# Performance work log

Hardware: AMD Instinct MI355X
Metric: run time of the kernel (lower is better)

Reference implementation:

```python
import jax, jax.numpy as jnp
import numpy as np

DIM = 512; H = 8; DH = 64; M = 256; ITERS = 6; K = 33  # residual conv kernel


def _pinv(x, iters=ITERS):
    # Moore-Penrose iterative pseudo-inverse (lucidrains moore_penrose_iter_pinv)
    abs_x = jnp.abs(x)
    denom = abs_x.sum(-1).max() * abs_x.sum(-2).max()  # global max of col/row sums
    z = jnp.swapaxes(x, -1, -2) / denom
    I = jnp.eye(x.shape[-1], dtype=x.dtype)
    for _ in range(iters):
        xz = x @ z
        z = 0.25 * z @ (13. * I - xz @ (15. * I - xz @ (7. * I - xz)))
    return z


def setup_inputs() -> dict:
    key = jax.random.key(0)
    ks = jax.random.split(key, 5)
    b, n = 4, 4096
    inner = H * DH
    x = jax.random.normal(ks[0], (b, n, DIM), jnp.float32)
    ln_g = jnp.ones((DIM,), jnp.float32)
    ln_b = jnp.zeros((DIM,), jnp.float32)
    w_qkv = jax.random.normal(ks[1], (DIM, 3 * inner), jnp.float32) / np.sqrt(DIM).astype(np.float32)
    w_out = jax.random.normal(ks[2], (inner, DIM), jnp.float32) / np.sqrt(inner).astype(np.float32)
    b_out = jnp.zeros((DIM,), jnp.float32)
    res_w = jax.random.normal(ks[3], (H, K), jnp.float32) * 0.02  # depthwise conv weight per head
    return {"x": x, "ln_g": ln_g, "ln_b": ln_b, "w_qkv": w_qkv,
            "w_out": w_out, "b_out": b_out, "res_w": res_w}


def reference(x, ln_g, ln_b, w_qkv, w_out, b_out, res_w):
    b, n, d = x.shape
    # LayerNorm (eps=1e-5, biased variance, like torch)
    mu = x.mean(-1, keepdims=True)
    var = ((x - mu) ** 2).mean(-1, keepdims=True)
    xn = (x - mu) * jax.lax.rsqrt(var + 1e-5) * ln_g + ln_b
    # QKV projection, no bias
    qkv = xn @ w_qkv  # [b, n, 3*h*dh]
    q, k, v = jnp.split(qkv, 3, axis=-1)
    tohd = lambda t: t.reshape(b, n, H, DH).transpose(0, 2, 1, 3)  # b h n d
    q = tohd(q) * (DH ** -0.5)
    k = tohd(k)
    v = tohd(v)
    # landmarks: mean over consecutive blocks of l = n // M (n divisible by M here)
    l = n // M
    q_l = q.reshape(b, H, M, l, DH).mean(3)  # b h m d
    k_l = k.reshape(b, H, M, l, DH).mean(3)
    attn1 = jax.nn.softmax(jnp.einsum('bhid,bhjd->bhij', q, k_l), axis=-1)   # b h n m
    attn2 = jax.nn.softmax(jnp.einsum('bhid,bhjd->bhij', q_l, k_l), axis=-1)  # b h m m
    attn3 = jax.nn.softmax(jnp.einsum('bhid,bhjd->bhij', q_l, k), axis=-1)   # b h m n
    out = (attn1 @ _pinv(attn2)) @ (attn3 @ v)  # b h n dh
    # depthwise residual conv over sequence dim (Conv2d(heads, heads, (33,1), groups=heads))
    res = jax.lax.conv_general_dilated(
        v, res_w.reshape(H, 1, K, 1), (1, 1), ((K // 2, K // 2), (0, 0)),
        feature_group_count=H, dimension_numbers=('NCHW', 'OIHW', 'NCHW'))
    out = out + res
    # merge heads + output projection (dropout is identity at eval)
    out = out.transpose(0, 2, 1, 3).reshape(b, n, H * DH) @ w_out + b_out
    # TransLayer residual
    return x + out
```

## Files before the change

kernel.cpp:

```cpp
#include <hip/hip_runtime.h>
#include <hip/hip_bf16.h>

#define SEQ    4096
#define NBAT   4
#define NHEAD  8
#define NBH    32
#define DMODEL 512
#define DHEAD  64
#define NLM    256
#define NSP    4

typedef __attribute__((ext_vector_type(8))) short s8v;
typedef __attribute__((ext_vector_type(4))) float f4v;

__device__ __forceinline__ float b2f(unsigned short u){
  union { unsigned int i; float f; } v; v.i = ((unsigned int)u) << 16; return v.f;
}
__device__ __forceinline__ unsigned short f2b(float f){
  union { float f; unsigned int i; } v; v.f = f;
  unsigned int r = v.i + 0x7fffu + ((v.i >> 16) & 1u);
  return (unsigned short)(r >> 16);
}
__device__ __forceinline__ s8v ldg8(const unsigned short* p){
  return *reinterpret_cast<const s8v*>(p);
}
__device__ __forceinline__ f4v mfma16(s8v a, s8v b, f4v c){
  return __builtin_amdgcn_mfma_f32_16x16x32_bf16(a, b, c, 0, 0, 0);
}
__device__ __forceinline__ f4v zero4(){ f4v z; z[0]=0.f; z[1]=0.f; z[2]=0.f; z[3]=0.f; return z; }
__device__ __forceinline__ void gload16(const unsigned short* g, unsigned short* l){
  __builtin_amdgcn_global_load_lds((const __attribute__((address_space(1))) unsigned int*)g,
                                   (__attribute__((address_space(3))) unsigned int*)l, 16, 0, 0);
}

__global__ void k_prep(const float* __restrict__ wqkv, const float* __restrict__ wout,
                       unsigned short* __restrict__ wqkvT, unsigned short* __restrict__ woutT,
                       unsigned int* __restrict__ denomU){
  int t = blockIdx.x*256 + threadIdx.x;
  if (t == 0) denomU[0] = 0u;
  if (t < 786432){ int kk = t/1536, n = t%1536; wqkvT[(size_t)n*512 + kk] = f2b(wqkv[t]); }
  else { int t2 = t - 786432; if (t2 < 262144){ int kk = t2/512, n = t2%512; woutT[(size_t)n*512 + kk] = f2b(wout[t2]); } }
}

__global__ __launch_bounds__(256) void k_ln(const float* __restrict__ x, const float* __restrict__ g,
                                            const float* __restrict__ be, unsigned short* __restrict__ xn){
  int row = blockIdx.x*4 + (threadIdx.x>>6);
  int l = threadIdx.x & 63;
  const float* xr = x + (size_t)row*DMODEL;
  float4 a = *(const float4*)(xr + l*4);
  float4 b = *(const float4*)(xr + 256 + l*4);
  float s = a.x+a.y+a.z+a.w + b.x+b.y+b.z+b.w;
  float q = a.x*a.x+a.y*a.y+a.z*a.z+a.w*a.w + b.x*b.x+b.y*b.y+b.z*b.z+b.w*b.w;
  #pragma unroll
  for (int m=1;m<64;m<<=1){ s += __shfl_xor(s,m); q += __shfl_xor(q,m); }
  float mean = s*(1.f/DMODEL);
  float rstd = rsqrtf(q*(1.f/DMODEL) - mean*mean + 1e-5f);
  int c0 = l*4, c1 = 256 + l*4;
  float av[4] = {a.x,a.y,a.z,a.w}, bv[4] = {b.x,b.y,b.z,b.w};
  ushort4 u0, u1;
  unsigned short* p0 = (unsigned short*)&u0; unsigned short* p1 = (unsigned short*)&u1;
  #pragma unroll
  for (int e=0;e<4;++e){
    p0[e] = f2b((av[e]-mean)*rstd*g[c0+e] + be[c0+e]);
    p1[e] = f2b((bv[e]-mean)*rstd*g[c1+e] + be[c1+e]);
  }
  *(ushort4*)(xn + (size_t)row*DMODEL + c0) = u0;
  *(ushort4*)(xn + (size_t)row*DMODEL + c1) = u1;
}

__device__ __forceinline__ void gemm512v2(const unsigned short* __restrict__ A, const unsigned short* __restrict__ B,
                                          int m0, int n0, int t, unsigned short* lA, unsigned short* lB,
                                          f4v acc[4][4]){
  int w = t>>6, l = t&63;
  int wm = (w&1)*64, wn = (w>>1)*64;
  int g = l>>4, qi = l&15;
  int rs = (w<<4) + (l>>2);
  int s0 = l&3;
  int c0 = ((s0 ^ ((rs>>1)&3)) << 3);
  int r1 = rs + 64;
  int c1 = ((s0 ^ ((r1>>1)&3)) << 3);
  const unsigned short* gA0 = A + (size_t)(m0+rs)*DMODEL + c0;
  const unsigned short* gA1 = A + (size_t)(m0+r1)*DMODEL + c1;
  const unsigned short* gB0 = B + (size_t)(n0+rs)*DMODEL + c0;
  const unsigned short* gB1 = B + (size_t)(n0+r1)*DMODEL + c1;
  unsigned short* dA0 = lA + (w<<9);
  unsigned short* dA1 = lA + 2048 + (w<<9);
  unsigned short* dB0 = lB + (w<<9);
  unsigned short* dB1 = lB + 2048 + (w<<9);
  int aofs[4], bofs[4];
  #pragma unroll
  for (int i=0;i<4;++i){
    int ra = wm + i*16 + qi;
    aofs[i] = ra*32 + ((g ^ ((ra>>1)&3))<<3);
    int rb = wn + i*16 + qi;
    bofs[i] = rb*32 + ((g ^ ((rb>>1)&3))<<3);
  }
  for (int ks=0; ks<16; ++ks){
    gload16(gA0, dA0); gload16(gA1, dA1);
    gload16(gB0, dB0); gload16(gB1, dB1);
    gA0 += 32; gA1 += 32; gB0 += 32; gB1 += 32;
    __syncthreads();
    s8v af[4], bf[4];
    #pragma unroll
    for (int i=0;i<4;++i) af[i] = *(s8v*)&lA[aofs[i]];
    #pragma unroll
    for (int j=0;j<4;++j) bf[j] = *(s8v*)&lB[bofs[j]];
    #pragma unroll
    for (int i=0;i<4;++i)
      #pragma unroll
      for (int j=0;j<4;++j) acc[i][j] = mfma16(af[i], bf[j], acc[i][j]);
    __syncthreads();
  }
}

__global__ __launch_bounds__(256) void k_gqkv(const unsigned short* __restrict__ xn, const unsigned short* __restrict__ wT,
                                              unsigned short* __restrict__ q, unsigned short* __restrict__ k,
                                              unsigned short* __restrict__ v, unsigned short* __restrict__ vT){
  __shared__ __align__(16) unsigned short lA[4096], lB[4096];
  int b0 = blockIdx.x;
  int bid = (b0 & 7) * 192 + (b0 >> 3);
  int mblk = bid/12, nblk = bid%12;
  int m0 = mblk*128, n0 = nblk*128;
  int t = threadIdx.x;
  f4v acc[4][4];
  #pragma unroll
  for (int i=0;i<4;++i)
    #pragma unroll
    for (int j=0;j<4;++j) acc[i][j] = zero4();
  gemm512v2(xn, wT, m0, n0, t, lA, lB, acc);
  int w = t>>6, l = t&63; int wm = (w&1)*64, wn = (w>>1)*64;
  int part = nblk >> 2;
  int coff = (nblk & 3) * 128;
  unsigned short* dst = (part==0) ? q : (part==1) ? k : v;
  float scale = (part==0) ? 0.125f : 1.f;
  #pragma unroll
  for (int i=0;i<4;++i)
  #pragma unroll
  for (int j=0;j<4;++j){
    int colg = coff + wn + j*16 + (l&15);
    int h = colg>>6, c = colg&63;
    #pragma unroll
    for (int r=0;r<4;++r){
      int rowg = m0 + wm + i*16 + ((l>>4)<<2) + r;
      int b = rowg>>12, n = rowg&4095;
      unsigned short val = f2b(acc[i][j][r]*scale);
      dst[ (((size_t)(b*NHEAD + h))*SEQ + n)*DHEAD + c ] = val;
      if (part == 2)
        vT[ (((size_t)(b*NHEAD + h))*DHEAD + c)*SEQ + n ] = val;
    }
  }
}

__global__ __launch_bounds__(256) void k_gout(const unsigned short* __restrict__ ao, const unsigned short* __restrict__ wT,
                                              const float* __restrict__ x, const float* __restrict__ bo,
                                              float* __restrict__ out){
  __shared__ __align__(16) unsigned short lA[4096], lB[4096];
  int b0 = blockIdx.x;
  int bid = (b0 & 7) * 64 + (b0 >> 3);
  int mblk = bid>>2, nblk = bid&3;
  int m0 = mblk*128, n0 = nblk*128;
  int t = threadIdx.x;
  f4v acc[4][4];
  #pragma unroll
  for (int i=0;i<4;++i)
    #pragma unroll
    for (int j=0;j<4;++j) acc[i][j] = zero4();
  gemm512v2(ao, wT, m0, n0, t, lA, lB, acc);
  int w = t>>6, l = t&63; int wm = (w&1)*64, wn = (w>>1)*64;
  #pragma unroll
  for (int i=0;i<4;++i)
  #pragma unroll
  for (int j=0;j<4;++j){
    int colg = n0 + wn + j*16 + (l&15);
    #pragma unroll
    for (int r=0;r<4;++r){
      int rowg = m0 + wm + i*16 + ((l>>4)<<2) + r;
      size_t ad = (size_t)rowg*DMODEL + colg;
      out[ad] = acc[i][j][r] + x[ad] + bo[colg];
    }
  }
}

__global__ void k_lmk(const unsigned short* __restrict__ q, const unsigned short* __restrict__ k,
                      unsigned short* __restrict__ ql, unsigned short* __restrict__ kl){
  int tg = blockIdx.x*256 + threadIdx.x;
  int c4 = (tg&15)*4, m = (tg>>4)&255, bh = tg>>12;
  const unsigned short* qb = q + ((size_t)bh*SEQ + m*16)*DHEAD + c4;
  const unsigned short* kb = k + ((size_t)bh*SEQ + m*16)*DHEAD + c4;
  float s0=0.f,s1=0.f,s2=0.f,s3=0.f, t0=0.f,t1=0.f,t2=0.f,t3=0.f;
  #pragma unroll
  for (int j=0;j<16;++j){
    ushort4 uq = *(const ushort4*)(qb + (size_t)j*DHEAD);
    ushort4 uk = *(const ushort4*)(kb + (size_t)j*DHEAD);
    s0+=b2f(uq.x); s1+=b2f(uq.y); s2+=b2f(uq.z); s3+=b2f(uq.w);
    t0+=b2f(uk.x); t1+=b2f(uk.y); t2+=b2f(uk.z); t3+=b2f(uk.w);
  }
  ushort4 oq, ok;
  oq.x=f2b(s0*(1.f/16.f)); oq.y=f2b(s1*(1.f/16.f)); oq.z=f2b(s2*(1.f/16.f)); oq.w=f2b(s3*(1.f/16.f));
  ok.x=f2b(t0*(1.f/16.f)); ok.y=f2b(t1*(1.f/16.f)); ok.z=f2b(t2*(1.f/16.f)); ok.w=f2b(t3*(1.f/16.f));
  *(ushort4*)(ql + ((size_t)bh*NLM + m)*DHEAD + c4) = oq;
  *(ushort4*)(kl + ((size_t)bh*NLM + m)*DHEAD + c4) = ok;
}

__global__ __launch_bounds__(512) void k_attn2(const unsigned short* __restrict__ ql, const unsigned short* __restrict__ kl,
                                               unsigned short* __restrict__ a2, unsigned short* __restrict__ a2t,
                                               unsigned int* __restrict__ denomU){
  __shared__ float cs[256];
  int bh = blockIdx.x; int t = threadIdx.x; int w = t>>6, l = t&63;
  const unsigned short* Q = ql + (size_t)bh*NLM*DHEAD;
  const unsigned short* K = kl + (size_t)bh*NLM*DHEAD;
  f4v acc[2][16];
  #pragma unroll
  for (int i=0;i<2;++i)
    #pragma unroll
    for (int j=0;j<16;++j) acc[i][j] = zero4();
  int m0 = w*32;
  #pragma unroll
  for (int ks=0; ks<2; ++ks){
    int kk = ks*32 + ((l>>4)<<3);
    s8v af0 = ldg8(&Q[(size_t)(m0 + (l&15))*DHEAD + kk]);
    s8v af1 = ldg8(&Q[(size_t)(m0 + 16 + (l&15))*DHEAD + kk]);
    #pragma unroll
    for (int j=0;j<16;++j){
      s8v bf = ldg8(&K[(size_t)(j*16 + (l&15))*DHEAD + kk]);
      acc[0][j] = mfma16(af0, bf, acc[0][j]);
      acc[1][j] = mfma16(af1, bf, acc[1][j]);
    }
  }
  #pragma unroll
  for (int i=0;i<2;++i)
  #pragma unroll
  for (int r=0;r<4;++r){
    float mx = -1e30f;
    #pragma unroll
    for (int j=0;j<16;++j) mx = fmaxf(mx, acc[i][j][r]);
    #pragma unroll
    for (int mm=1;mm<16;mm<<=1) mx = fmaxf(mx, __shfl_xor(mx,mm));
    float sm = 0.f;
    #pragma unroll
    for (int j=0;j<16;++j){ float p = __expf(acc[i][j][r]-mx); acc[i][j][r]=p; sm += p; }
    #pragma unroll
    for (int mm=1;mm<16;mm<<=1) sm += __shfl_xor(sm,mm);
    float inv = 1.f/sm;
    #pragma unroll
    for (int j=0;j<16;++j) acc[i][j][r] *= inv;
  }
  for (int e=t; e<256; e+=512) cs[e] = 0.f;
  __syncthreads();
  size_t b0 = (size_t)bh*NLM*NLM;
  #pragma unroll
  for (int i=0;i<2;++i)
  #pragma unroll
  for (int j=0;j<16;++j){
    int col = j*16 + (l&15);
    int rowb = m0 + i*16 + ((l>>4)<<2);
    float csp = 0.f;
    #pragma unroll
    for (int r=0;r<4;++r){
      float p = acc[i][j][r];
      unsigned short pb = f2b(p);
      a2 [b0 + (size_t)(rowb+r)*NLM + col] = pb;
      a2t[b0 + (size_t)col*NLM + rowb + r] = pb;
      csp += p;
    }
    csp += __shfl_xor(csp, 16); csp += __shfl_xor(csp, 32);
    if ((l>>4) == 0) atomicAdd(&cs[col], csp);
  }
  __syncthreads();
  if (t < 256) atomicMax(denomU, __float_as_uint(cs[t]));
}

__global__ __launch_bounds__(128) void k_a3w2p(const unsigned short* __restrict__ ql, const unsigned short* __restrict__ kb,
                                               const unsigned short* __restrict__ vT,
                                               float* __restrict__ po, float* __restrict__ pm, float* __restrict__ pd){
  int ksp = blockIdx.x & 3;
  int qb  = (blockIdx.x >> 2) & 7;
  int bh  = blockIdx.x >> 5;
  int t = threadIdx.x, w = t>>6, l = t&63;
  int q0 = (qb<<5) + (w<<4);
  int g = l>>4, qi = l&15;
  const unsigned short* Q = ql + ((size_t)bh*NLM + q0)*DHEAD;
  const unsigned short* K = kb + (size_t)bh*SEQ*DHEAD;
  const unsigned short* V = vT + (size_t)bh*DHEAD*SEQ;
  float m_run = -1e30f, den = 0.f;
  f4v oacc[4];
  #pragma unroll
  for (int j=0;j<4;++j) oacc[j] = zero4();
  int sl0 = ((g&1)*2)*16 + qi;
  int jsel = g>>1;
  for (int kc = ksp*4; kc < ksp*4+4; ++kc){
    const unsigned short* Kc = K + (size_t)kc*256*DHEAD;
    f4v acc[16];
    #pragma unroll
    for (int j=0;j<16;++j) acc[j] = zero4();
    #pragma unroll
    for (int ks=0;ks<2;++ks){
      int kk = ks*32 + g*8;
      s8v bq = ldg8(&Q[(size_t)qi*DHEAD + kk]);
      #pragma unroll
      for (int j=0;j<16;++j){
        s8v ak = ldg8(&Kc[(size_t)(j*16+qi)*DHEAD + kk]);
        acc[j] = mfma16(ak, bq, acc[j]);
      }
    }
    float cm = -1e30f;
    #pragma unroll
    for (int j=0;j<16;++j)
      cm = fmaxf(cm, fmaxf(fmaxf(acc[j][0],acc[j][1]), fmaxf(acc[j][2],acc[j][3])));
    cm = fmaxf(cm, __shfl_xor(cm,16));
    cm = fmaxf(cm, __shfl_xor(cm,32));
    float nm = fmaxf(m_run, cm);
    float f = __expf(m_run - nm);
    m_run = nm;
    float ls = 0.f;
    unsigned int pku[32];
    #pragma unroll
    for (int j=0;j<16;++j){
      float p0 = __expf(acc[j][0]-nm), p1 = __expf(acc[j][1]-nm);
      float p2 = __expf(acc[j][2]-nm), p3 = __expf(acc[j][3]-nm);
      ls += (p0+p1)+(p2+p3);
      pku[2*j+0] = (unsigned int)f2b(p0) | ((unsigned int)f2b(p1)<<16);
      pku[2*j+1] = (unsigned int)f2b(p2) | ((unsigned int)f2b(p3)<<16);
    }
    den = den*f + ls;
    float fr0 = __shfl(f, g*4+0, 64), fr1 = __shfl(f, g*4+1, 64);
    float fr2 = __shfl(f, g*4+2, 64), fr3 = __shfl(f, g*4+3, 64);
    #pragma unroll
    for (int j=0;j<4;++j){
      oacc[j][0]*=fr0; oacc[j][1]*=fr1; oacc[j][2]*=fr2; oacc[j][3]*=fr3;
    }
    #pragma unroll
    for (int ks=0;ks<8;++ks){
      unsigned int w0a = (unsigned int)__shfl((int)pku[4*ks+0], sl0, 64);
      unsigned int w1a = (unsigned int)__shfl((int)pku[4*ks+1], sl0, 64);
      unsigned int w0b = (unsigned int)__shfl((int)pku[4*ks+2], sl0, 64);
      unsigned int w1b = (unsigned int)__shfl((int)pku[4*ks+3], sl0, 64);
      unsigned int w2a = (unsigned int)__shfl((int)pku[4*ks+0], sl0+16, 64);
      unsigned int w3a = (unsigned int)__shfl((int)pku[4*ks+1], sl0+16, 64);
      unsigned int w2b = (unsigned int)__shfl((int)pku[4*ks+2], sl0+16, 64);
      unsigned int w3b = (unsigned int)__shfl((int)pku[4*ks+3], sl0+16, 64);
      unsigned int wv0 = jsel ? w0b : w0a;
      unsigned int wv1 = jsel ? w1b : w1a;
      unsigned int wv2 = jsel ? w2b : w2a;
      unsigned int wv3 = jsel ? w3b : w3a;
      s8v af;
      af[0] = (short)(wv0&0xffff); af[1] = (short)(wv0>>16);
      af[2] = (short)(wv1&0xffff); af[3] = (short)(wv1>>16);
      af[4] = (short)(wv2&0xffff); af[5] = (short)(wv2>>16);
      af[6] = (short)(wv3&0xffff); af[7] = (short)(wv3>>16);
      int mk = ks*32 + g*8;
      #pragma unroll
      for (int j=0;j<4;++j){
        s8v bu = ldg8(&V[(size_t)(j*16+qi)*SEQ + kc*256 + mk]);
        oacc[j] = mfma16(af, bu, oacc[j]);
      }
    }
  }
  den += __shfl_xor(den,16); den += __shfl_xor(den,32);
  #pragma unroll
  for (int j=0;j<4;++j)
    #pragma unroll
    for (int r=0;r<4;++r)
      po[(((size_t)(ksp*NBH + bh))*NLM + q0 + g*4 + r)*DHEAD + j*16 + qi] = oacc[j][r];
  if (g == 0){
    pm[(size_t)(ksp*NBH + bh)*NLM + q0 + qi] = m_run;
    pd[(size_t)(ksp*NBH + bh)*NLM + q0 + qi] = den;
  }
}

__global__ __launch_bounds__(256) void k_a3c(const float* __restrict__ po, const float* __restrict__ pm,
                                             const float* __restrict__ pd, unsigned short* __restrict__ w2t){
  int tg = blockIdx.x*256 + threadIdx.x;
  int bh = tg >> 12; int c = (tg >> 6) & 63; int r4 = (tg & 63) << 2;
  ushort4 ov;
  unsigned short* op = (unsigned short*)&ov;
  #pragma unroll
  for (int rr=0; rr<4; ++rr){
    int row = r4 + rr;
    float m[NSP];
    float gm = -1e30f;
    #pragma unroll
    for (int s=0;s<NSP;++s){ m[s] = pm[(size_t)(s*NBH+bh)*NLM + row]; gm = fmaxf(gm, m[s]); }
    float den = 0.f, o = 0.f;
    #pragma unroll
    for (int s=0;s<NSP;++s){
      float wsc = __expf(m[s]-gm);
      den += pd[(size_t)(s*NBH+bh)*NLM + row]*wsc;
      o   += po[(((size_t)(s*NBH+bh))*NLM + row)*DHEAD + c]*wsc;
    }
    op[rr] = f2b(o/den);
  }
  *(ushort4*)&w2t[(size_t)bh*DHEAD*NLM + (size_t)c*NLM + r4] = ov;
}

__global__ __launch_bounds__(256) void k_conv(const unsigned short* __restrict__ v, const float* __restrict__ rw,
                                              unsigned short* __restrict__ cf){
  int bh = blockIdx.x >> 6;
  int n0 = (blockIdx.x & 63) * 64;
  int h = bh & 7, b = bh >> 3;
  int t = threadIdx.x;
  int tx = t & 15, ty = t >> 4;
  int c4 = tx * 4;
  int nb = n0 + ty * 4;
  const unsigned short* vb = v + ((size_t)bh * SEQ) * DHEAD + c4;
  ushort4 val[36];
  #pragma unroll
  for (int i = 0; i < 36; ++i){
    int nn = nb - 16 + i;
    if (nn >= 0 && nn < SEQ) val[i] = *(const ushort4*)(vb + (size_t)nn * DHEAD);
    else { val[i].x = 0; val[i].y = 0; val[i].z = 0; val[i].w = 0; }
  }
  float wgt[33];
  #pragma unroll
  for (int o = 0; o < 33; ++o) wgt[o] = rw[h*33 + o];
  #pragma unroll
  for (int i = 0; i < 4; ++i){
    float s0 = 0.f, s1 = 0.f, s2 = 0.f, s3 = 0.f;
    #pragma unroll
    for (int o = 0; o < 33; ++o){
      ushort4 u = val[i + o];
      float w0 = wgt[o];
      s0 += w0 * b2f(u.x); s1 += w0 * b2f(u.y);
      s2 += w0 * b2f(u.z); s3 += w0 * b2f(u.w);
    }
    ushort4 ov;
    ov.x = f2b(s0); ov.y = f2b(s1); ov.z = f2b(s2); ov.w = f2b(s3);
    size_t ad = ((size_t)b * SEQ + (nb + i)) * DMODEL + h * DHEAD + c4;
    *(ushort4*)(cf + ad) = ov;
  }
}

__device__ __forceinline__ void pcore(const unsigned short* __restrict__ Ab, const unsigned short* __restrict__ Bb,
                                      int m0, int n0, int l, f4v acc[4][4]){
  for (int ks=0; ks<8; ++ks){
    int kk = ks*32 + ((l>>4)<<3);
    s8v af[4], bf[4];
    #pragma unroll
    for (int i=0;i<4;++i) af[i] = ldg8(&Ab[(size_t)(m0 + i*16 + (l&15))*256 + kk]);
    #pragma unroll
    for (int j=0;j<4;++j) bf[j] = ldg8(&Bb[(size_t)(n0 + j*16 + (l&15))*256 + kk]);
    #pragma unroll
    for (int i=0;i<4;++i)
      #pragma unroll
      for (int j=0;j<4;++j) acc[i][j] = mfma16(af[i], bf[j], acc[i][j]);
  }
}

__global__ __launch_bounds__(64) void k_pg1(const unsigned short* __restrict__ A, const unsigned short* __restrict__ BT,
                                            unsigned short* __restrict__ oN, unsigned short* __restrict__ oT,
                                            int sdiv, const unsigned int* __restrict__ denomU){
  int bid = blockIdx.x;
  int bh = bid>>4, tt = bid&15;
  int m0 = (tt>>2)*64, n0 = (tt&3)*64;
  int l = threadIdx.x;
  const unsigned short* Ab = A + (size_t)bh*65536;
  const unsigned short* Bb = BT + (size_t)bh*65536;
  f4v acc[4][4];
  #pragma unroll
  for (int i=0;i<4;++i)
    #pragma unroll
    for (int j=0;j<4;++j) acc[i][j] = zero4();
  pcore(Ab, Bb, m0, n0, l, acc);
  float s = sdiv ? 1.f/__uint_as_float(denomU[0]) : 1.f;
  #pragma unroll
  for (int i=0;i<4;++i)
  #pragma unroll
  for (int j=0;j<4;++j){
    int col = n0 + j*16 + (l&15);
    #pragma unroll
    for (int r=0;r<4;++r){
      int row = m0 + i*16 + ((l>>4)<<2) + r;
      unsigned short ob = f2b(acc[i][j][r]*s);
      oN[(size_t)bh*65536 + (size_t)row*256 + col] = ob;
      oT[(size_t)bh*65536 + (size_t)col*256 + row] = ob;
    }
  }
}

__global__ __launch_bounds__(64) void k_pg2(const unsigned short* __restrict__ xzN, const unsigned short* __restrict__ xzT,
                                            const unsigned short* __restrict__ zsrc,
                                            unsigned short* __restrict__ CT, unsigned short* __restrict__ PN,
                                            int sdiv, const unsigned int* __restrict__ denomU){
  int bid = blockIdx.x;
  int part = bid>>9; bid &= 511;
  int bh = bid>>4, tt = bid&15;
  int m0 = (tt>>2)*64, n0 = (tt&3)*64;
  int l = threadIdx.x;
  const unsigned short* Ab = (part==0 ? xzN : zsrc) + (size_t)bh*65536;
  const unsigned short* Bb = xzT + (size_t)bh*65536;
  f4v acc[4][4];
  #pragma unroll
  for (int i=0;i<4;++i)
    #pragma unroll
    for (int j=0;j<4;++j) acc[i][j] = zero4();
  pcore(Ab, Bb, m0, n0, l, acc);
  if (part == 0){
    #pragma unroll
    for (int i=0;i<4;++i)
    #pragma unroll
    for (int j=0;j<4;++j){
      int col = n0 + j*16 + (l&15);
      #pragma unroll
      for (int r=0;r<4;++r){
        int row = m0 + i*16 + ((l>>4)<<2) + r;
        float xv = b2f(xzN[(size_t)bh*65536 + (size_t)row*256 + col]);
        CT[(size_t)bh*65536 + (size_t)col*256 + row] = f2b(7.f*xv - acc[i][j][r]);
      }
    }
  } else {
    float s = sdiv ? 1.f/__uint_as_float(denomU[0]) : 1.f;
    #pragma unroll
    for (int i=0;i<4;++i)
    #pragma unroll
    for (int j=0;j<4;++j){
      int col = n0 + j*16 + (l&15);
      #pragma unroll
      for (int r=0;r<4;++r){
        int row = m0 + i*16 + ((l>>4)<<2) + r;
        PN[(size_t)bh*65536 + (size_t)row*256 + col] = f2b(acc[i][j][r]*s);
      }
    }
  }
}

__global__ __launch_bounds__(64) void k_pg3(const unsigned short* __restrict__ PN, const unsigned short* __restrict__ CT,
                                            const unsigned short* __restrict__ zsrc,
                                            unsigned short* __restrict__ zN, unsigned short* __restrict__ zT,
                                            int sdiv, const unsigned int* __restrict__ denomU){
  int bid = blockIdx.x;
  int bh = bid>>4, tt = bid&15;
  int m0 = (tt>>2)*64, n0 = (tt&3)*64;
  int l = threadIdx.x;
  const unsigned short* Ab = PN + (size_t)bh*65536;
  const unsigned short* Bb = CT + (size_t)bh*65536;
  f4v acc[4][4];
  #pragma unroll
  for (int i=0;i<4;++i)
    #pragma unroll
    for (int j=0;j<4;++j) acc[i][j] = zero4();
  pcore(Ab, Bb, m0, n0, l, acc);
  float zs = sdiv ? 1.f/__uint_as_float(denomU[0]) : 1.f;
  #pragma unroll
  for (int i=0;i<4;++i)
  #pragma unroll
  for (int j=0;j<4;++j){
    int col = n0 + j*16 + (l&15);
    #pragma unroll
    for (int r=0;r<4;++r){
      int row = m0 + i*16 + ((l>>4)<<2) + r;
      float zv = b2f(zsrc[(size_t)bh*65536 + (size_t)row*256 + col])*zs;
      float pv = b2f(PN  [(size_t)bh*65536 + (size_t)row*256 + col]);
      float res = 0.25f*(13.f*zv - 15.f*pv + acc[i][j][r]);
      unsigned short ob = f2b(res);
      zN[(size_t)bh*65536 + (size_t)row*256 + col] = ob;
      zT[(size_t)bh*65536 + (size_t)col*256 + row] = ob;
    }
  }
}

template<bool WN, bool WT>
__global__ __launch_bounds__(64) void k_pgemm(
    const unsigned short* __restrict__ A, const unsigned short* __restrict__ BT,
    unsigned short* __restrict__ oN, unsigned short* __restrict__ oT,
    int mt, int nt, long strA, long strBT, long strON, long strOT)
{
  int bid = blockIdx.x;
  int nper = mt*nt;
  int bh = bid/nper, tt = bid%nper;
  int m0 = (tt/nt)*64, n0 = (tt%nt)*64;
  const unsigned short* Ab = A + (size_t)bh*strA;
  const unsigned short* Bb = BT + (size_t)bh*strBT;
  int l = threadIdx.x;
  f4v acc[4][4];
  #pragma unroll
  for (int i=0;i<4;++i)
    #pragma unroll
    for (int j=0;j<4;++j) acc[i][j] = zero4();
  pcore(Ab, Bb, m0, n0, l, acc);
  #pragma unroll
  for (int i=0;i<4;++i)
  #pragma unroll
  for (int j=0;j<4;++j){
    int col = n0 + j*16 + (l&15);
    #pragma unroll
    for (int r=0;r<4;++r){
      int row = m0 + i*16 + ((l>>4)<<2) + r;
      unsigned short ob = f2b(acc[i][j][r]);
      if constexpr (WN) oN[(size_t)bh*strON + (size_t)row*256 + col] = ob;
      if constexpr (WT) oT[(size_t)bh*strOT + (size_t)col*256 + row] = ob;
    }
  }
}

__global__ __launch_bounds__(256) void k_attn1(const unsigned short* __restrict__ qb, const unsigned short* __restrict__ kl,
                                               const unsigned short* __restrict__ ut, const unsigned short* __restrict__ cf,
                                               unsigned short* __restrict__ ao){
  int bh = blockIdx.x>>6;
  int t = threadIdx.x, w = t>>6, l = t&63;
  int q0 = ((blockIdx.x&63)<<6) + (w<<4);
  int g = l>>4, qi = l&15;
  const unsigned short* Q = qb + (size_t)bh*SEQ*DHEAD;
  const unsigned short* K = kl + (size_t)bh*NLM*DHEAD;
  f4v acc[16];
  #pragma unroll
  for (int j=0;j<16;++j) acc[j] = zero4();
  #pragma unroll
  for (int ks=0;ks<2;++ks){
    int kk = ks*32 + g*8;
    s8v bq = ldg8(&Q[(size_t)(q0+qi)*DHEAD + kk]);
    #pragma unroll
    for (int j=0;j<16;++j){
      s8v ak = ldg8(&K[(size_t)(j*16+qi)*DHEAD + kk]);
      acc[j] = mfma16(ak, bq, acc[j]);
    }
  }
  float mx = -1e30f;
  #pragma unroll
  for (int j=0;j<16;++j)
    mx = fmaxf(mx, fmaxf(fmaxf(acc[j][0],acc[j][1]), fmaxf(acc[j][2],acc[j][3])));
  mx = fmaxf(mx, __shfl_xor(mx,16));
  mx = fmaxf(mx, __shfl_xor(mx,32));
  float sm = 0.f;
  #pragma unroll
  for (int j=0;j<16;++j)
    #pragma unroll
    for (int r=0;r<4;++r){ float p = __expf(acc[j][r]-mx); acc[j][r]=p; sm += p; }
  sm += __shfl_xor(sm,16); sm += __shfl_xor(sm,32);
  float inv = 1.f/sm;
  unsigned int pku[32];
  #pragma unroll
  for (int j=0;j<16;++j){
    pku[2*j+0] = (unsigned int)f2b(acc[j][0]*inv) | ((unsigned int)f2b(acc[j][1]*inv)<<16);
    pku[2*j+1] = (unsigned int)f2b(acc[j][2]*inv) | ((unsigned int)f2b(acc[j][3]*inv)<<16);
  }
  const unsigned short* U = ut + (size_t)bh*DHEAD*NLM;
  f4v oacc[4];
  #pragma unroll
  for (int j=0;j<4;++j) oacc[j] = zero4();
  int sl0 = ((g&1)*2)*16 + qi;
  int jsel = g>>1;
  #pragma unroll
  for (int ks=0;ks<8;++ks){
    unsigned int w0a = (unsigned int)__shfl((int)pku[4*ks+0], sl0, 64);
    unsigned int w1a = (unsigned int)__shfl((int)pku[4*ks+1], sl0, 64);
    unsigned int w0b = (unsigned int)__shfl((int)pku[4*ks+2], sl0, 64);
    unsigned int w1b = (unsigned int)__shfl((int)pku[4*ks+3], sl0, 64);
    unsigned int w2a = (unsigned int)__shfl((int)pku[4*ks+0], sl0+16, 64);
    unsigned int w3a = (unsigned int)__shfl((int)pku[4*ks+1], sl0+16, 64);
    unsigned int w2b = (unsigned int)__shfl((int)pku[4*ks+2], sl0+16, 64);
    unsigned int w3b = (unsigned int)__shfl((int)pku[4*ks+3], sl0+16, 64);
    unsigned int wv0 = jsel ? w0b : w0a;
    unsigned int wv1 = jsel ? w1b : w1a;
    unsigned int wv2 = jsel ? w2b : w2a;
    unsigned int wv3 = jsel ? w3b : w3a;
    s8v af;
    af[0] = (short)(wv0&0xffff); af[1] = (short)(wv0>>16);
    af[2] = (short)(wv1&0xffff); af[3] = (short)(wv1>>16);
    af[4] = (short)(wv2&0xffff); af[5] = (short)(wv2>>16);
    af[6] = (short)(wv3&0xffff); af[7] = (short)(wv3>>16);
    int mk = ks*32 + g*8;
    #pragma unroll
    for (int j=0;j<4;++j){
      s8v bu = ldg8(&U[(size_t)(j*16+qi)*NLM + mk]);
      oacc[j] = mfma16(af, bu, oacc[j]);
    }
  }
  int b = bh>>3, h = bh&7;
  #pragma unroll
  for (int j=0;j<4;++j){
    int c = j*16 + qi;
    #pragma unroll
    for (int r=0;r<4;++r){
      int n = q0 + g*4 + r;
      size_t ad = ((size_t)(b*SEQ + n))*DMODEL + h*DHEAD + c;
      ao[ad] = f2b(oacc[j][r] + b2f(cf[ad]));
    }
  }
}

extern "C" void kernel_launch(void* const* d_in, const int* in_sizes, int n_in,
                              void* d_out, int out_size, void* d_ws, size_t ws_size,
                              hipStream_t stream){
  const float* x    = (const float*)d_in[0];
  const float* lng  = (const float*)d_in[1];
  const float* lnb  = (const float*)d_in[2];
  const float* wqkv = (const float*)d_in[3];
  const float* wout = (const float*)d_in[4];
  const float* bout = (const float*)d_in[5];
  const float* resw = (const float*)d_in[6];
  float* out = (float*)d_out;

  char* ws = (char*)d_ws;
  size_t off = 0;
  auto alloc = [&](size_t bytes)->char*{ char* p = ws + off; off += (bytes + 255) & ~(size_t)255; return p; };

  unsigned short* wqkvT = (unsigned short*)alloc((size_t)1536*512*2);
  unsigned short* woutT = (unsigned short*)alloc((size_t)512*512*2);
  unsigned int*   denomU= (unsigned int*)  alloc(256);
  unsigned short* xn    = (unsigned short*)alloc((size_t)16384*512*2);
  unsigned short* zA  = xn;
  unsigned short* zAT = xn + (size_t)1*NBH*NLM*NLM;
  unsigned short* zB  = xn + (size_t)2*NBH*NLM*NLM;
  unsigned short* zBT = xn + (size_t)3*NBH*NLM*NLM;
  unsigned short* q   = (unsigned short*)alloc((size_t)NBH*SEQ*DHEAD*2);
  unsigned short* kb  = (unsigned short*)alloc((size_t)NBH*SEQ*DHEAD*2);
  unsigned short* ao  = kb;
  unsigned short* v   = (unsigned short*)alloc((size_t)NBH*SEQ*DHEAD*2);
  unsigned short* vT  = (unsigned short*)alloc((size_t)NBH*DHEAD*SEQ*2);
  unsigned short* ql  = (unsigned short*)alloc((size_t)NBH*NLM*DHEAD*2);
  unsigned short* kl  = (unsigned short*)alloc((size_t)NBH*NLM*DHEAD*2);
  unsigned short* a2  = (unsigned short*)alloc((size_t)NBH*NLM*NLM*2);
  unsigned short* a2t = (unsigned short*)alloc((size_t)NBH*NLM*NLM*2);
  unsigned short* convf = (unsigned short*)alloc((size_t)NBAT*SEQ*DMODEL*2);
  unsigned short* xzN = (unsigned short*)alloc((size_t)NBH*NLM*NLM*2);
  unsigned short* xzT = (unsigned short*)alloc((size_t)NBH*NLM*NLM*2);
  unsigned short* pn  = (unsigned short*)alloc((size_t)NBH*NLM*NLM*2);
  unsigned short* ctb = (unsigned short*)alloc((size_t)NBH*NLM*NLM*2);
  float* po = (float*)alloc((size_t)NSP*NBH*NLM*DHEAD*4);
  float* pm = (float*)alloc((size_t)NSP*NBH*NLM*4);
  float* pd = (float*)alloc((size_t)NSP*NBH*NLM*4);
  unsigned short* w2t = (unsigned short*)alloc((size_t)NBH*DHEAD*NLM*2);
  unsigned short* ut  = (unsigned short*)alloc((size_t)NBH*DHEAD*NLM*2);
  (void)ws_size; (void)in_sizes; (void)n_in; (void)out_size;

  k_prep<<<4096,256,0,stream>>>(wqkv, wout, wqkvT, woutT, denomU);
  k_ln  <<<4096,256,0,stream>>>(x, lng, lnb, xn);
  k_gqkv<<<1536,256,0,stream>>>(xn, wqkvT, q, kb, v, vT);
  k_lmk <<<512,256,0,stream>>>(q, kb, ql, kl);
  k_attn2<<<32,512,0,stream>>>(ql, kl, a2, a2t, denomU);
  k_a3w2p<<<1024,128,0,stream>>>(ql, kb, vT, po, pm, pd);
  k_a3c <<<512,256,0,stream>>>(po, pm, pd, w2t);
  k_conv<<<2048,256,0,stream>>>(v, resw, convf);

  unsigned short* zN_[2] = {zA, zB};
  unsigned short* zT_[2] = {zAT, zBT};
  for (int it = 0; it < 6; ++it){
    const unsigned short* BT   = (it==0) ? a2  : zT_[(it-1)&1];
    const unsigned short* zsrc = (it==0) ? a2t : zN_[(it-1)&1];
    int sdiv = (it==0) ? 1 : 0;
    k_pg1<<<512 ,64,0,stream>>>(a2, BT, xzN, xzT, sdiv, denomU);
    k_pg2<<<1024,64,0,stream>>>(xzN, xzT, zsrc, ctb, pn, sdiv, denomU);
    k_pg3<<<512 ,64,0,stream>>>(pn, ctb, zsrc, zN_[it&1], zT_[it&1], sdiv, denomU);
  }
  k_pgemm<false,true><<<128,64,0,stream>>>(zN_[1], w2t, (unsigned short*)nullptr, ut, 4,1, 65536L,16384L,0L,16384L);

  k_attn1<<<2048,256,0,stream>>>(q, kl, ut, convf, ao);
  k_gout <<<512,256,0,stream>>>(ao, woutT, x, bout, out);
}
```

Before: 497.1 us.

## Fuse pseudo-inverse iterations into one persistent kernel with grid barriers

Replaces the 18 per-iteration GEMM launches plus the final pgemm with a single persistent kernel of 512 blocks that synchronises through atomic-counter grid barriers in global memory. The two GEMMs that were split across 1024 blocks in pg2 are now done back to back by each block. The goal is to remove launch overhead and inter-kernel gaps in the small serial Newton-Schulz chain. In exchange, each block does twice the work in one phase, and the spin barriers rely on all 512 blocks being co-resident, risking deadlock otherwise.

Measured after the change: 1.570 ms. 3.16x slower.

```diff
diff --git a/kernel.cpp b/kernel.cpp
--- a/kernel.cpp
+++ b/kernel.cpp
@@ -35,9 +35,10 @@
 
 __global__ void k_prep(const float* __restrict__ wqkv, const float* __restrict__ wout,
                        unsigned short* __restrict__ wqkvT, unsigned short* __restrict__ woutT,
-                       unsigned int* __restrict__ denomU){
+                       unsigned int* __restrict__ denomU, unsigned int* __restrict__ bar){
   int t = blockIdx.x*256 + threadIdx.x;
   if (t == 0) denomU[0] = 0u;
+  if (t < 64) bar[t] = 0u;
   if (t < 786432){ int kk = t/1536, n = t%1536; wqkvT[(size_t)n*512 + kk] = f2b(wqkv[t]); }
   else { int t2 = t - 786432; if (t2 < 262144){ int kk = t2/512, n = t2%512; woutT[(size_t)n*512 + kk] = f2b(wout[t2]); } }
 }
@@ -446,148 +447,146 @@
   }
 }
 
-__global__ __launch_bounds__(64) void k_pg1(const unsigned short* __restrict__ A, const unsigned short* __restrict__ BT,
-                                            unsigned short* __restrict__ oN, unsigned short* __restrict__ oT,
-                                            int sdiv, const unsigned int* __restrict__ denomU){
+__device__ __forceinline__ void gbar(unsigned int* __restrict__ bar, int ph, int l){
+  __threadfence();
+  if (l == 0) atomicAdd(&bar[ph], 1u);
+  while (__hip_atomic_load(&bar[ph], __ATOMIC_RELAXED, __HIP_MEMORY_SCOPE_AGENT) < 512u)
+    __builtin_amdgcn_s_sleep(8);
+  __threadfence();
+}
+
+__global__ __launch_bounds__(64) void k_pinv(
+    const unsigned short* __restrict__ a2, const unsigned short* __restrict__ a2t,
+    const unsigned short* __restrict__ w2t, unsigned short* __restrict__ ut,
+    unsigned short* __restrict__ xzN, unsigned short* __restrict__ xzT,
+    unsigned short* __restrict__ ctb, unsigned short* __restrict__ pn,
+    unsigned short* __restrict__ zA, unsigned short* __restrict__ zAT,
+    unsigned short* __restrict__ zB, unsigned short* __restrict__ zBT,
+    const unsigned int* __restrict__ denomU, unsigned int* __restrict__ bar)
+{
   int bid = blockIdx.x;
+  int l = threadIdx.x;
   int bh = bid>>4, tt = bid&15;
   int m0 = (tt>>2)*64, n0 = (tt&3)*64;
-  int l = threadIdx.x;
-  const unsigned short* Ab = A + (size_t)bh*65536;
-  const unsigned short* Bb = BT + (size_t)bh*65536;
-  f4v acc[4][4];
-  #pragma unroll
-  for (int i=0;i<4;++i)
-    #pragma unroll
-    for (int j=0;j<4;++j) acc[i][j] = zero4();
-  pcore(Ab, Bb, m0, n0, l, acc);
-  float s = sdiv ? 1.f/__uint_as_float(denomU[0]) : 1.f;
-  #pragma unroll
-  for (int i=0;i<4;++i)
-  #pragma unroll
-  for (int j=0;j<4;++j){
-    int col = n0 + j*16 + (l&15);
-    #pragma unroll
-    for (int r=0;r<4;++r){
-      int row = m0 + i*16 + ((l>>4)<<2) + r;
-      unsigned short ob = f2b(acc[i][j][r]*s);
-      oN[(size_t)bh*65536 + (size_t)row*256 + col] = ob;
-      oT[(size_t)bh*65536 + (size_t)col*256 + row] = ob;
-    }
-  }
-}
-
-__global__ __launch_bounds__(64) void k_pg2(const unsigned short* __restrict__ xzN, const unsigned short* __restrict__ xzT,
-                                            const unsigned short* __restrict__ zsrc,
-                                            unsigned short* __restrict__ CT, unsigned short* __restrict__ PN,
-                                            int sdiv, const unsigned int* __restrict__ denomU){
-  int bid = blockIdx.x;
-  int part = bid>>9; bid &= 511;
-  int bh = bid>>4, tt = bid&15;
-  int m0 = (tt>>2)*64, n0 = (tt&3)*64;
-  int l = threadIdx.x;
-  const unsigned short* Ab = (part==0 ? xzN : zsrc) + (size_t)bh*65536;
-  const unsigned short* Bb = xzT + (size_t)bh*65536;
-  f4v acc[4][4];
-  #pragma unroll
-  for (int i=0;i<4;++i)
-    #pragma unroll
-    for (int j=0;j<4;++j) acc[i][j] = zero4();
-  pcore(Ab, Bb, m0, n0, l, acc);
-  if (part == 0){
+  size_t bb = (size_t)bh*65536;
+  float dinv = 1.f/__uint_as_float(denomU[0]);
+  unsigned short* zN_[2] = {zA, zB};
+  unsigned short* zT_[2] = {zAT, zBT};
+  int ph = 0;
+  for (int it=0; it<6; ++it){
+    const unsigned short* BT   = (it==0) ? a2  : zT_[(it-1)&1];
+    const unsigned short* zsrc = (it==0) ? a2t : zN_[(it-1)&1];
+    float s = (it==0) ? dinv : 1.f;
+    {
+      f4v acc[4][4];
+      #pragma unroll
+      for (int i=0;i<4;++i)
+        #pragma unroll
+        for (int j=0;j<4;++j) acc[i][j] = zero4();
+      pcore(a2+bb, BT+bb, m0, n0, l, acc);
+      #pragma unroll
+      for (int i=0;i<4;++i)
+      #pragma unroll
+      for (int j=0;j<4;++j){
+        int col = n0 + j*16 + (l&15);
+        #pragma unroll
+        for (int r=0;r<4;++r){
+          int row = m0 + i*16 + ((l>>4)<<2) + r;
+          unsigned short ob = f2b(acc[i][j][r]*s);
+          xzN[bb + (size_t)row*256 + col] = ob;
+          xzT[bb + (size_t)col*256 + row] = ob;
+        }
+      }
+    }
+    gbar(bar, ph++, l);
+    {
+      f4v acc[4][4];
+      #pragma unroll
+      for (int i=0;i<4;++i)
+        #pragma unroll
+        for (int j=0;j<4;++j) acc[i][j] = zero4();
+      pcore(xzN+bb, xzT+bb, m0, n0, l, acc);
+      #pragma unroll
+      for (int i=0;i<4;++i)
+      #pragma unroll
+      for (int j=0;j<4;++j){
+        int col = n0 + j*16 + (l&15);
+        #pragma unroll
+        for (int r=0;r<4;++r){
+          int row = m0 + i*16 + ((l>>4)<<2) + r;
+          float xv = b2f(xzN[bb + (size_t)row*256 + col]);
+          ctb[bb + (size_t)col*256 + row] = f2b(7.f*xv - acc[i][j][r]);
+        }
+      }
+    }
+    {
+      f4v acc[4][4];
+      #pragma unroll
+      for (int i=0;i<4;++i)
+        #pragma unroll
+        for (int j=0;j<4;++j) acc[i][j] = zero4();
+      pcore(zsrc+bb, xzT+bb, m0, n0, l, acc);
+      #pragma unroll
+      for (int i=0;i<4;++i)
+      #pragma unroll
+      for (int j=0;j<4;++j){
+        int col = n0 + j*16 + (l&15);
+        #pragma unroll
+        for (int r=0;r<4;++r){
+          int row = m0 + i*16 + ((l>>4)<<2) + r;
+          pn[bb + (size_t)row*256 + col] = f2b(acc[i][j][r]*s);
+        }
+      }
+    }
+    gbar(bar, ph++, l);
+    {
+      f4v acc[4][4];
+      #pragma unroll
+      for (int i=0;i<4;++i)
+        #pragma unroll
+        for (int j=0;j<4;++j) acc[i][j] = zero4();
+      pcore(pn+bb, ctb+bb, m0, n0, l, acc);
+      unsigned short* zdN = zN_[it&1];
+      unsigned short* zdT = zT_[it&1];
+      #pragma unroll
+      for (int i=0;i<4;++i)
+      #pragma unroll
+      for (int j=0;j<4;++j){
+        int col = n0 + j*16 + (l&15);
+        #pragma unroll
+        for (int r=0;r<4;++r){
+          int row = m0 + i*16 + ((l>>4)<<2) + r;
+          size_t idx = bb + (size_t)row*256 + col;
+          float zv = b2f(zsrc[idx])*s;
+          float pv = b2f(pn[idx]);
+          float res = 0.25f*(13.f*zv - 15.f*pv + acc[i][j][r]);
+          unsigned short ob = f2b(res);
+          zdN[idx] = ob;
+          zdT[bb + (size_t)col*256 + row] = ob;
+        }
+      }
+    }
+    gbar(bar, ph++, l);
+  }
+  if (bid < 128){
+    int bh2 = bid>>2, tte = bid&3;
+    int m0e = tte*64;
+    f4v acc[4][4];
     #pragma unroll
     for (int i=0;i<4;++i)
+      #pragma unroll
+      for (int j=0;j<4;++j) acc[i][j] = zero4();
+    pcore(zB + (size_t)bh2*65536, w2t + (size_t)bh2*16384, m0e, 0, l, acc);
+    #pragma unroll
+    for (int i=0;i<4;++i)
     #pragma unroll
     for (int j=0;j<4;++j){
-      int col = n0 + j*16 + (l&15);
+      int col = j*16 + (l&15);
       #pragma unroll
       for (int r=0;r<4;++r){
-        int row = m0 + i*16 + ((l>>4)<<2) + r;
-        float xv = b2f(xzN[(size_t)bh*65536 + (size_t)row*256 + col]);
-        CT[(size_t)bh*65536 + (size_t)col*256 + row] = f2b(7.f*xv - acc[i][j][r]);
+        int row = m0e + i*16 + ((l>>4)<<2) + r;
+        ut[(size_t)bh2*16384 + (size_t)col*256 + row] = f2b(acc[i][j][r]);
       }
-    }
-  } else {
-    float s = sdiv ? 1.f/__uint_as_float(denomU[0]) : 1.f;
-    #pragma unroll
-    for (int i=0;i<4;++i)
-    #pragma unroll
-    for (int j=0;j<4;++j){
-      int col = n0 + j*16 + (l&15);
-      #pragma unroll
-      for (int r=0;r<4;++r){
-        int row = m0 + i*16 + ((l>>4)<<2) + r;
-        PN[(size_t)bh*65536 + (size_t)row*256 + col] = f2b(acc[i][j][r]*s);
-      }
-    }
-  }
-}
-
-__global__ __launch_bounds__(64) void k_pg3(const unsigned short* __restrict__ PN, const unsigned short* __restrict__ CT,
-                                            const unsigned short* __restrict__ zsrc,
-                                            unsigned short* __restrict__ zN, unsigned short* __restrict__ zT,
-                                            int sdiv, const unsigned int* __restrict__ denomU){
-  int bid = blockIdx.x;
-  int bh = bid>>4, tt = bid&15;
-  int m0 = (tt>>2)*64, n0 = (tt&3)*64;
-  int l = threadIdx.x;
-  const unsigned short* Ab = PN + (size_t)bh*65536;
-  const unsigned short* Bb = CT + (size_t)bh*65536;
-  f4v acc[4][4];
-  #pragma unroll
-  for (int i=0;i<4;++i)
-    #pragma unroll
-    for (int j=0;j<4;++j) acc[i][j] = zero4();
-  pcore(Ab, Bb, m0, n0, l, acc);
-  float zs = sdiv ? 1.f/__uint_as_float(denomU[0]) : 1.f;
-  #pragma unroll
-  for (int i=0;i<4;++i)
-  #pragma unroll
-  for (int j=0;j<4;++j){
-    int col = n0 + j*16 + (l&15);
-    #pragma unroll
-    for (int r=0;r<4;++r){
-      int row = m0 + i*16 + ((l>>4)<<2) + r;
-      float zv = b2f(zsrc[(size_t)bh*65536 + (size_t)row*256 + col])*zs;
-      float pv = b2f(PN  [(size_t)bh*65536 + (size_t)row*256 + col]);
-      float res = 0.25f*(13.f*zv - 15.f*pv + acc[i][j][r]);
-      unsigned short ob = f2b(res);
-      zN[(size_t)bh*65536 + (size_t)row*256 + col] = ob;
-      zT[(size_t)bh*65536 + (size_t)col*256 + row] = ob;
-    }
-  }
-}
-
-template<bool WN, bool WT>
-__global__ __launch_bounds__(64) void k_pgemm(
-    const unsigned short* __restrict__ A, const unsigned short* __restrict__ BT,
-    unsigned short* __restrict__ oN, unsigned short* __restrict__ oT,
-    int mt, int nt, long strA, long strBT, long strON, long strOT)
-{
-  int bid = blockIdx.x;
-  int nper = mt*nt;
-  int bh = bid/nper, tt = bid%nper;
-  int m0 = (tt/nt)*64, n0 = (tt%nt)*64;
-  const unsigned short* Ab = A + (size_t)bh*strA;
-  const unsigned short* Bb = BT + (size_t)bh*strBT;
-  int l = threadIdx.x;
-  f4v acc[4][4];
-  #pragma unroll
-  for (int i=0;i<4;++i)
-    #pragma unroll
-    for (int j=0;j<4;++j) acc[i][j] = zero4();
-  pcore(Ab, Bb, m0, n0, l, acc);
-  #pragma unroll
-  for (int i=0;i<4;++i)
-  #pragma unroll
-  for (int j=0;j<4;++j){
-    int col = n0 + j*16 + (l&15);
-    #pragma unroll
-    for (int r=0;r<4;++r){
-      int row = m0 + i*16 + ((l>>4)<<2) + r;
-      unsigned short ob = f2b(acc[i][j][r]);
-      if constexpr (WN) oN[(size_t)bh*strON + (size_t)row*256 + col] = ob;
-      if constexpr (WT) oT[(size_t)bh*strOT + (size_t)col*256 + row] = ob;
     }
   }
 }
@@ -697,6 +696,7 @@
   unsigned short* wqkvT = (unsigned short*)alloc((size_t)1536*512*2);
   unsigned short* woutT = (unsigned short*)alloc((size_t)512*512*2);
   unsigned int*   denomU= (unsigned int*)  alloc(256);
+  unsigned int*   bar   = (unsigned int*)  alloc(256);
   unsigned short* xn    = (unsigned short*)alloc((size_t)16384*512*2);
   unsigned short* zA  = xn;
   unsigned short* zAT = xn + (size_t)1*NBH*NLM*NLM;
@@ -723,7 +723,7 @@
   unsigned short* ut  = (unsigned short*)alloc((size_t)NBH*DHEAD*NLM*2);
   (void)ws_size; (void)in_sizes; (void)n_in; (void)out_size;
 
-  k_prep<<<4096,256,0,stream>>>(wqkv, wout, wqkvT, woutT, denomU);
+  k_prep<<<4096,256,0,stream>>>(wqkv, wout, wqkvT, woutT, denomU, bar);
   k_ln  <<<4096,256,0,stream>>>(x, lng, lnb, xn);
   k_gqkv<<<1536,256,0,stream>>>(xn, wqkvT, q, kb, v, vT);
   k_lmk <<<512,256,0,stream>>>(q, kb, ql, kl);
@@ -732,17 +732,7 @@
   k_a3c <<<512,256,0,stream>>>(po, pm, pd, w2t);
   k_conv<<<2048,256,0,stream>>>(v, resw, convf);
 
-  unsigned short* zN_[2] = {zA, zB};
-  unsigned short* zT_[2] = {zAT, zBT};
-  for (int it = 0; it < 6; ++it){
-    const unsigned short* BT   = (it==0) ? a2  : zT_[(it-1)&1];
-    const unsigned short* zsrc = (it==0) ? a2t : zN_[(it-1)&1];
-    int sdiv = (it==0) ? 1 : 0;
-    k_pg1<<<512 ,64,0,stream>>>(a2, BT, xzN, xzT, sdiv, denomU);
-    k_pg2<<<1024,64,0,stream>>>(xzN, xzT, zsrc, ctb, pn, sdiv, denomU);
-    k_pg3<<<512 ,64,0,stream>>>(pn, ctb, zsrc, zN_[it&1], zT_[it&1], sdiv, denomU);
-  }
-  k_pgemm<false,true><<<128,64,0,stream>>>(zN_[1], w2t, (unsigned short*)nullptr, ut, 4,1, 65536L,16384L,0L,16384L);
+  k_pinv<<<512,64,0,stream>>>(a2, a2t, w2t, ut, xzN, xzT, ctb, pn, zA, zAT, zB, zBT, denomU, bar);
 
   k_attn1<<<2048,256,0,stream>>>(q, kl, ut, convf, ao);
   k_gout <<<512,256,0,stream>>>(ao, woutT, x, bout, out);
```

## Stage K and V chunks in swizzled LDS shared by four waves in k_a3w2p

Applied to the files above, without the earlier changes.

The attn3·V partial kernel now uses 256-thread blocks covering 64 landmark queries instead of 128-thread blocks covering 32. Each 256-key chunk of K and V is loaded once per block into XOR-swizzled shared memory with direct global-to-LDS loads, and each wave reads its MFMA operands from there instead of global memory. The Q fragments are also loaded once before the key loop. This halves redundant K/V global/L2 traffic, but adds two barriers per chunk with no double buffering, so load latency is exposed, and 64KB of LDS per block may limit occupancy.

After: 459.0 us. -7.7%, faster.

```diff
diff --git a/kernel.cpp b/kernel.cpp
--- a/kernel.cpp
+++ b/kernel.cpp
@@ -270,18 +270,23 @@
   if (t < 256) atomicMax(denomU, __float_as_uint(cs[t]));
 }
 
-__global__ __launch_bounds__(128) void k_a3w2p(const unsigned short* __restrict__ ql, const unsigned short* __restrict__ kb,
+__global__ __launch_bounds__(256) void k_a3w2p(const unsigned short* __restrict__ ql, const unsigned short* __restrict__ kb,
                                                const unsigned short* __restrict__ vT,
                                                float* __restrict__ po, float* __restrict__ pm, float* __restrict__ pd){
-  int ksp = blockIdx.x & 3;
-  int qb  = (blockIdx.x >> 2) & 7;
-  int bh  = blockIdx.x >> 5;
+  __shared__ __align__(16) unsigned short Ks[256*64];
+  __shared__ __align__(16) unsigned short Vs[64*256];
+  int bid = blockIdx.x;
+  int ksp = bid & 3;
+  int qp  = (bid >> 2) & 3;
+  int bh  = bid >> 4;
   int t = threadIdx.x, w = t>>6, l = t&63;
-  int q0 = (qb<<5) + (w<<4);
+  int q0 = qp*64 + w*16;
   int g = l>>4, qi = l&15;
   const unsigned short* Q = ql + ((size_t)bh*NLM + q0)*DHEAD;
   const unsigned short* K = kb + (size_t)bh*SEQ*DHEAD;
   const unsigned short* V = vT + (size_t)bh*DHEAD*SEQ;
+  s8v bq0 = ldg8(&Q[(size_t)qi*DHEAD + g*8]);
+  s8v bq1 = ldg8(&Q[(size_t)qi*DHEAD + 32 + g*8]);
   float m_run = -1e30f, den = 0.f;
   f4v oacc[4];
   #pragma unroll
@@ -290,16 +295,25 @@
   int jsel = g>>1;
   for (int kc = ksp*4; kc < ksp*4+4; ++kc){
     const unsigned short* Kc = K + (size_t)kc*256*DHEAD;
+    #pragma unroll
+    for (int it2=0; it2<8; ++it2){
+      int cid = it2*256 + t;
+      int row = cid>>3, cl = cid&7;
+      gload16(&Kc[(size_t)(row<<6) + ((cl^(row&7))<<3)], Ks + it2*2048 + w*512);
+      int row2 = cid>>5, cl2 = cid&31;
+      gload16(&V[(size_t)row2*SEQ + kc*256 + ((cl2^(row2&7))<<3)], Vs + it2*2048 + 16384 - 16384 + w*512 + 0);
+    }
+    __syncthreads();
     f4v acc[16];
     #pragma unroll
     for (int j=0;j<16;++j) acc[j] = zero4();
     #pragma unroll
     for (int ks=0;ks<2;++ks){
-      int kk = ks*32 + g*8;
-      s8v bq = ldg8(&Q[(size_t)qi*DHEAD + kk]);
+      s8v bq = (ks==0) ? bq0 : bq1;
       #pragma unroll
       for (int j=0;j<16;++j){
-        s8v ak = ldg8(&Kc[(size_t)(j*16+qi)*DHEAD + kk]);
+        int r = j*16+qi;
+        s8v ak = *(s8v*)&Ks[(size_t)(r<<6) + (((ks*4+g) ^ (qi&7))<<3)];
         acc[j] = mfma16(ak, bq, acc[j]);
       }
     }
@@ -348,13 +362,15 @@
       af[2] = (short)(wv1&0xffff); af[3] = (short)(wv1>>16);
       af[4] = (short)(wv2&0xffff); af[5] = (short)(wv2>>16);
       af[6] = (short)(wv3&0xffff); af[7] = (short)(wv3>>16);
-      int mk = ks*32 + g*8;
+      int ch = ks*4 + g;
       #pragma unroll
       for (int j=0;j<4;++j){
-        s8v bu = ldg8(&V[(size_t)(j*16+qi)*SEQ + kc*256 + mk]);
+        int r = j*16+qi;
+        s8v bu = *(s8v*)&Vs[(size_t)(r<<8) + ((ch ^ (qi&7))<<3)];
         oacc[j] = mfma16(af, bu, oacc[j]);
       }
     }
+    __syncthreads();
   }
   den += __shfl_xor(den,16); den += __shfl_xor(den,32);
   #pragma unroll
@@ -728,7 +744,7 @@
   k_gqkv<<<1536,256,0,stream>>>(xn, wqkvT, q, kb, v, vT);
   k_lmk <<<512,256,0,stream>>>(q, kb, ql, kl);
   k_attn2<<<32,512,0,stream>>>(ql, kl, a2, a2t, denomU);
-  k_a3w2p<<<1024,128,0,stream>>>(ql, kb, vT, po, pm, pd);
+  k_a3w2p<<<512,256,0,stream>>>(ql, kb, vT, po, pm, pd);
   k_a3c <<<512,256,0,stream>>>(po, pm, pd, w2t);
   k_conv<<<2048,256,0,stream>>>(v, resw, convf);
 
```
